# Performance work log

Measured on AMD Instinct MI355X. Metric: run time of the kernel, lower is better.

The kernel has to match this reference:

```python
import jax, jax.numpy as jnp
import numpy as np
from jax import lax

# SparseLSTM(input_size=1024, hidden_size=1024, blocks=4, density=0.5)
# input segments: width 512 at starts [0,170,341,512] (overlapping)
# output segments: contiguous quarters of 256
K = 4
IB = 512   # per-block input width
HB = 256   # per-block hidden width
STARTS = (0, 170, 341, 512)


def setup_inputs() -> dict:
    key = jax.random.key(0)
    ks = jax.random.split(key, 8)
    T, B, D = 512, 64, 1024
    std = 1.0 / np.sqrt(HB)
    return {
        "x":  jax.random.normal(ks[0], (T, B, D), jnp.float32),
        "h0": jax.random.normal(ks[1], (1, B, D), jnp.float32),
        "c0": jax.random.normal(ks[2], (1, B, D), jnp.float32),
        # stacked per-block LSTM params, PyTorch gate order (i, f, g, o)
        "W_ih": jax.random.uniform(ks[3], (K, 4 * HB, IB), jnp.float32, -std, std),
        "W_hh": jax.random.uniform(ks[4], (K, 4 * HB, HB), jnp.float32, -std, std),
        "b_ih": jax.random.uniform(ks[5], (K, 4 * HB), jnp.float32, -std, std),
        "b_hh": jax.random.uniform(ks[6], (K, 4 * HB), jnp.float32, -std, std),
    }


def _sparse_lstm(x, h0, c0, W_ih, W_hh, b_ih, b_hh):
    T, B, _ = x.shape
    # gather overlapping input slices -> [k, T, B, IB]
    xb = jnp.stack([lax.slice_in_dim(x, s, s + IB, axis=2) for s in STARTS])
    # contiguous hidden quarters -> [k, B, HB]
    hb = h0[0].reshape(B, K, HB).transpose(1, 0, 2)
    cb = c0[0].reshape(B, K, HB).transpose(1, 0, 2)
    # precompute input contributions to gates: [T, k, B, 4*HB]
    xg = jnp.einsum("ktbi,kgi->tkbg", xb, W_ih) + (b_ih + b_hh)[None, :, None, :]

    def step(carry, xg_t):
        h, c = carry  # each [k, B, HB]
        gates = xg_t + jnp.einsum("kbh,kgh->kbg", h, W_hh)
        i, f, g, o = jnp.split(gates, 4, axis=-1)
        c = jax.nn.sigmoid(f) * c + jax.nn.sigmoid(i) * jnp.tanh(g)
        h = jax.nn.sigmoid(o) * jnp.tanh(c)
        return (h, c), h

    (hT, cT), ys = lax.scan(step, (hb, cb), xg)  # ys: [T, k, B, HB]
    output = ys.transpose(0, 2, 1, 3).reshape(T, B, K * HB)
    new_h = hT.transpose(1, 0, 2).reshape(B, K * HB)[None]
    new_c = cT.transpose(1, 0, 2).reshape(B, K * HB)[None]
    return output, new_h, new_c


def reference(x, h0, c0, W_ih, W_hh, b_ih, b_hh):
    return _sparse_lstm(x, h0, c0, W_ih, W_hh, b_ih, b_hh)
```

## Files before the change

### kernel.cpp

```cpp
#include <hip/hip_runtime.h>

typedef _Float16 half8   __attribute__((ext_vector_type(8)));
typedef _Float16 half2_t __attribute__((ext_vector_type(2)));
typedef float    floatx4 __attribute__((ext_vector_type(4)));
typedef unsigned int uintx4 __attribute__((ext_vector_type(4)));
typedef unsigned int uint32;

__device__ __forceinline__ float sigm(float v) { return 1.0f / (1.0f + __expf(-v)); }
__device__ __forceinline__ float tanh_(float v) { float e = __expf(2.0f * v); return (e - 1.0f) / (e + 1.0f); }

__device__ __forceinline__ int dot4(uint32 a, uint32 b, int c) {
#if __has_builtin(__builtin_amdgcn_sdot4)
  return __builtin_amdgcn_sdot4((int)a, (int)b, c, false);
#else
  int r = c;
  r += (int)(char)(a)       * (int)(char)(b);
  r += (int)(char)(a >> 8)  * (int)(char)(b >> 8);
  r += (int)(char)(a >> 16) * (int)(char)(b >> 16);
  r += (int)(char)(a >> 24) * (int)(char)(b >> 24);
  return r;
#endif
}

__device__ __forceinline__ uint32 pack_rte(float a, float b) {
  half2_t h; h[0] = (_Float16)a; h[1] = (_Float16)b;
  return __builtin_bit_cast(uint32, h);
}

__global__ __launch_bounds__(256) void pack_wih(const float* __restrict__ wih, uint32* __restrict__ wihd) {
  int p = blockIdx.x * 256 + threadIdx.x;
  wihd[p] = pack_rte(wih[2 * p], wih[2 * p + 1]);
}

__global__ __launch_bounds__(256) void pack_whh8(const float* __restrict__ whh, uintx4* __restrict__ wq8) {
  int p = blockIdx.x * 256 + threadIdx.x;
  int row = p & 1023, qi = (p >> 10) & 3, qt = (p >> 12) & 3, kk = p >> 14;
  const float* src = whh + ((size_t)(kk * 1024 + row)) * 256 + qt * 64 + qi * 16;
  uint32 dw[4];
#pragma unroll
  for (int d = 0; d < 4; ++d) {
    uint32 v = 0;
#pragma unroll
    for (int e = 0; e < 4; ++e) {
      int q = (int)rintf(src[d * 4 + e] * 2032.0f);
      q = q > 127 ? 127 : (q < -127 ? -127 : q);
      v |= ((uint32)(q & 0xff)) << (8 * e);
    }
    dw[d] = v;
  }
  wq8[p] = (uintx4){dw[0], dw[1], dw[2], dw[3]};
}

__global__ __launch_bounds__(256) void pack_x_all(const float* __restrict__ x, uint32* __restrict__ xsd) {
  for (long p = (long)blockIdx.x * 256 + threadIdx.x; p < 33554432L; p += 2097152L) {
    int chunk = (int)(p >> 21);
    int r = (int)(p & 2097151);
    int k  = r >> 19;
    int R  = (r >> 8) & 2047;
    int pc = r & 255;
    int b = R >> 5, ct = R & 31;
    int t = chunk * 32 + ct;
    int sk = (k * 1024) / 6;
    const float* src = x + ((size_t)t * 64 + b) * 1024 + sk + pc * 2;
    xsd[p] = pack_rte(src[0], src[1]);
  }
}

__global__ __launch_bounds__(256) void gemm_all(const _Float16* __restrict__ xs,
                                                const _Float16* __restrict__ wih16,
                                                const float* __restrict__ bih,
                                                const float* __restrict__ bhh,
                                                _Float16* __restrict__ xg) {
  __shared__ _Float16 SL[18432];
  const int tid = threadIdx.x;
  const int bid = blockIdx.x;
  const int chunk = bid >> 9;
  const int b9 = bid & 511;
  const int nt = b9 & 7, mt = (b9 >> 3) & 15, kb = b9 >> 7;
  const int l = tid & 63;
  const int wid = tid >> 6;
  const int wm = wid >> 1, wn = wid & 1;
  const int lr = l & 15, lk = l >> 4;

  floatx4 acc[4][4] = {};
  const _Float16* xsk = xs + ((size_t)(chunk * 4 + kb) << 20);
  const _Float16* wk  = wih16 + ((size_t)kb << 19);

  for (int kt = 0; kt < 8; ++kt) {
    const int K0 = kt * 64;
    half8 av[4], bv[4];
#pragma unroll
    for (int q = 0; q < 4; ++q) {
      int s = q * 256 + tid;
      int row = s >> 3, c8 = s & 7;
      av[q] = *(const half8*)(xsk + (size_t)(mt * 128 + row) * 512 + K0 + c8 * 8);
      bv[q] = *(const half8*)(wk  + (size_t)(nt * 128 + row) * 512 + K0 + c8 * 8);
    }
#pragma unroll
    for (int q = 0; q < 4; ++q) {
      int s = q * 256 + tid;
      int row = s >> 3, c8 = s & 7;
      *(half8*)&SL[row * 72 + c8 * 8]        = av[q];
      *(half8*)&SL[9216 + row * 72 + c8 * 8] = bv[q];
    }
    __syncthreads();
#pragma unroll
    for (int ks = 0; ks < 2; ++ks) {
      half8 af[4], bf[4];
#pragma unroll
      for (int fm = 0; fm < 4; ++fm)
        af[fm] = *(const half8*)&SL[(wm * 64 + fm * 16 + lr) * 72 + (ks * 4 + lk) * 8];
#pragma unroll
      for (int fn = 0; fn < 4; ++fn)
        bf[fn] = *(const half8*)&SL[9216 + (wn * 64 + fn * 16 + lr) * 72 + (ks * 4 + lk) * 8];
#pragma unroll
      for (int fm = 0; fm < 4; ++fm)
#pragma unroll
        for (int fn = 0; fn < 4; ++fn)
          acc[fm][fn] = __builtin_amdgcn_mfma_f32_16x16x32_f16(af[fm], bf[fn], acc[fm][fn], 0, 0, 0);
    }
    __syncthreads();
  }
  float bias[4];
#pragma unroll
  for (int fn = 0; fn < 4; ++fn) {
    int g = nt * 128 + wn * 64 + fn * 16 + lr;
    bias[fn] = bih[kb * 1024 + g] + bhh[kb * 1024 + g];
  }
#pragma unroll
  for (int fm = 0; fm < 4; ++fm)
#pragma unroll
    for (int fn = 0; fn < 4; ++fn) {
      int colb = wn * 64 + fn * 16 + lr;
#pragma unroll
      for (int r = 0; r < 4; ++r) {
        int rowb = wm * 64 + fm * 16 + lk * 4 + r;
        SL[rowb * 128 + colb] = (_Float16)(acc[fm][fn][r] + bias[fn]);
      }
    }
  __syncthreads();
#pragma unroll
  for (int q = 0; q < 8; ++q) {
    int s = q * 256 + tid;
    int row = s >> 4, c16 = s & 15;
    int R = mt * 128 + row;
    size_t off = ((size_t)(kb * 64 + (R >> 5)) * 512 + chunk * 32 + (R & 31)) * 1024 + nt * 128 + c16 * 8;
    *(uintx4*)(xg + off) = *(const uintx4*)&SL[row * 128 + c16 * 8];
  }
}

__global__ __attribute__((amdgpu_flat_work_group_size(256, 256), amdgpu_waves_per_eu(1, 1)))
void lstm_all(const _Float16* __restrict__ xg,
              const uintx4* __restrict__ wq8,
              const float* __restrict__ h0,
              const float* __restrict__ c0,
              float* __restrict__ out) {
  extern __shared__ uint32 lds[];
  unsigned char* h8   = (unsigned char*)lds;
  _Float16*      hist = (_Float16*)(lds + 128);
  const _Float16* slab = (const _Float16*)(lds + 4224);
  const int j = threadIdx.x;
  const int k = blockIdx.x >> 6, b = blockIdx.x & 63;

  const uintx4* wb = wq8 + ((size_t)k << 14);
#define LW(g, i) uintx4 W##g##_##i = wb[((i) >> 2) * 4096 + ((i) & 3) * 1024 + (g) * 256 + j];
#define LWG(g) LW(g,0) LW(g,1) LW(g,2) LW(g,3) LW(g,4) LW(g,5) LW(g,6) LW(g,7) \
               LW(g,8) LW(g,9) LW(g,10) LW(g,11) LW(g,12) LW(g,13) LW(g,14) LW(g,15)
  LWG(0) LWG(1) LWG(2) LWG(3)
#undef LW
#undef LWG

  const int gi = b * 1024 + k * 256 + j;
  float cst = c0[gi];
  float hlast = h0[gi];
  {
    int q = (int)rintf(hlast * (127.0f / 8.0f));
    q = q > 127 ? 127 : (q < -127 ? -127 : q);
    h8[j] = (unsigned char)(q & 0xff);
  }

  const float DS1 = 0.0625f / 16129.0f;
  const float DS8 = 8.0f * DS1;

  const _Float16* xgp = xg + ((size_t)(k * 64 + b) << 19);

#define MACQ(W, H, d) { d = dot4(W[0], H[0], d); d = dot4(W[1], H[1], d); \
                        d = dot4(W[2], H[2], d); d = dot4(W[3], H[3], d); }
#define QSTEP(i) { uintx4 hq = hp[i]; \
    MACQ(W0_##i, hq, d0) MACQ(W1_##i, hq, d1) MACQ(W2_##i, hq, d2) MACQ(W3_##i, hq, d3) }

#pragma unroll 1
  for (int t = 0; t < 512; ++t) {
    if ((t & 31) == 0) {
      if (t) {
        int tb = t - 32;
#pragma unroll 1
        for (int q = 0; q < 32; ++q)
          out[((size_t)(tb + q) * 64 + b) * 1024 + k * 256 + j] = (float)hist[q * 256 + j];
      }
#pragma unroll
      for (int q = 0; q < 16; ++q)
        __builtin_amdgcn_global_load_lds(
            (const __attribute__((address_space(1))) void*)(xgp + (size_t)t * 1024 + q * 2048 + j * 8),
            (__attribute__((address_space(3))) void*)(lds + 4224 + q * 1024 + j * 4), 16, 0, 0);
      asm volatile("s_waitcnt vmcnt(0)" ::: "memory");
      __builtin_amdgcn_sched_barrier(0);
      __syncthreads();
    }

    const int cur = t & 1;
    const uintx4* hp = (const uintx4*)(h8 + cur * 256);
    int d0 = 0, d1 = 0, d2 = 0, d3 = 0;
    QSTEP(0)  QSTEP(1)  QSTEP(2)  QSTEP(3)  QSTEP(4)  QSTEP(5)  QSTEP(6)  QSTEP(7)
    QSTEP(8)  QSTEP(9)  QSTEP(10) QSTEP(11) QSTEP(12) QSTEP(13) QSTEP(14) QSTEP(15)

    const int ts = (t & 31) * 1024;
    float xi = (float)slab[ts + j];
    float xf = (float)slab[ts + 256 + j];
    float xgv = (float)slab[ts + 512 + j];
    float xo = (float)slab[ts + 768 + j];

    float dsc = (t == 0) ? DS8 : DS1;
    float iv = (float)d0 * dsc + xi;
    float fv = (float)d1 * dsc + xf;
    float gv = (float)d2 * dsc + xgv;
    float ov = (float)d3 * dsc + xo;
    float cn = sigm(fv) * cst + sigm(iv) * tanh_(gv);
    float hn = sigm(ov) * tanh_(cn);
    cst = cn; hlast = hn;
    hist[(t & 31) * 256 + j] = (_Float16)hn;
    {
      int q = (int)rintf(hn * 127.0f);
      h8[(cur ^ 1) * 256 + j] = (unsigned char)(q & 0xff);
    }
    __syncthreads();
  }
#undef MACQ
#undef QSTEP

#pragma unroll 1
  for (int q = 0; q < 32; ++q)
    out[((size_t)(480 + q) * 64 + b) * 1024 + k * 256 + j] = (float)hist[q * 256 + j];
  out[33554432 + gi] = hlast;
  out[33554432 + 65536 + gi] = cst;
}

extern "C" void kernel_launch(void* const* d_in, const int* in_sizes, int n_in,
                              void* d_out, int out_size, void* d_ws, size_t ws_size,
                              hipStream_t stream) {
  const float* x   = (const float*)d_in[0];
  const float* h0  = (const float*)d_in[1];
  const float* c0  = (const float*)d_in[2];
  const float* Wih = (const float*)d_in[3];
  const float* Whh = (const float*)d_in[4];
  const float* bih = (const float*)d_in[5];
  const float* bhh = (const float*)d_in[6];
  float* out = (float*)d_out;
  char* ws = (char*)d_ws;

  _Float16* xg16  = (_Float16*)ws;
  _Float16* xs    = (_Float16*)(ws + 268435456L);
  _Float16* wih16 = (_Float16*)(ws + 402653184L);
  uintx4*   wq8   = (uintx4*)(ws + 406847488L);

  hipFuncSetAttribute((const void*)lstm_all, hipFuncAttributeMaxDynamicSharedMemorySize, 82432);

  pack_wih<<<4096, 256, 0, stream>>>(Wih, (uint32*)wih16);
  pack_whh8<<<256, 256, 0, stream>>>(Whh, wq8);
  pack_x_all<<<8192, 256, 0, stream>>>(x, (uint32*)xs);
  gemm_all<<<8192, 256, 0, stream>>>(xs, wih16, bih, bhh, xg16);
  lstm_all<<<256, 256, 82432, stream>>>(xg16, wq8, h0, c0, out);
}
```

Measured before the change: 1.190 ms.

## Move recurrent weights partly to LDS and double-buffer small xg slabs

The recurrent kernel now keeps only one gate's int8 weights in registers, stages two gates plus part of the third in LDS (156 KB) and streams the rest of the third gate from global/L2 every step. The input-gate slab changes from a 32-step bulk load to a 4-step double-buffered prefetch, and hidden outputs are written straight to global memory each step instead of being batched through an LDS history buffer. The aim is to cut register pressure and the stalls from periodic bulk loads and flushes. In exchange, every step adds LDS and global weight reads on the serial critical path.

After: 1.953 ms. 1.64x slower.

```diff
diff --git a/kernel.cpp b/kernel.cpp
--- a/kernel.cpp
+++ b/kernel.cpp
@@ -149,7 +149,7 @@
   }
 }
 
-__global__ __attribute__((amdgpu_flat_work_group_size(256, 256), amdgpu_waves_per_eu(1, 1)))
+__global__ __launch_bounds__(256, 1)
 void lstm_all(const _Float16* __restrict__ xg,
               const uintx4* __restrict__ wq8,
               const float* __restrict__ h0,
@@ -157,68 +157,90 @@
               float* __restrict__ out) {
   extern __shared__ uint32 lds[];
   unsigned char* h8   = (unsigned char*)lds;
-  _Float16*      hist = (_Float16*)(lds + 128);
-  const _Float16* slab = (const _Float16*)(lds + 4224);
+  _Float16*      slab = (_Float16*)(lds + 128);
+  uintx4*        wl4  = (uintx4*)(lds + 4224);
   const int j = threadIdx.x;
   const int k = blockIdx.x >> 6, b = blockIdx.x & 63;
 
-  const uintx4* wb = wq8 + ((size_t)k << 14);
-#define LW(g, i) uintx4 W##g##_##i = wb[((i) >> 2) * 4096 + ((i) & 3) * 1024 + (g) * 256 + j];
-#define LWG(g) LW(g,0) LW(g,1) LW(g,2) LW(g,3) LW(g,4) LW(g,5) LW(g,6) LW(g,7) \
-               LW(g,8) LW(g,9) LW(g,10) LW(g,11) LW(g,12) LW(g,13) LW(g,14) LW(g,15)
-  LWG(0) LWG(1) LWG(2) LWG(3)
-#undef LW
-#undef LWG
+  const uintx4* wk = wq8 + ((size_t)k << 14);
+#define LR(i) uintx4 R##i = wk[((i) >> 2) * 4096 + ((i) & 3) * 1024 + j];
+  LR(0) LR(1) LR(2) LR(3) LR(4) LR(5) LR(6) LR(7)
+  LR(8) LR(9) LR(10) LR(11) LR(12) LR(13) LR(14) LR(15)
+#undef LR
+#pragma unroll
+  for (int g = 1; g <= 2; ++g)
+#pragma unroll
+    for (int i = 0; i < 16; ++i)
+      wl4[((g - 1) * 16 + i) * 256 + j] = wk[(i >> 2) * 4096 + (i & 3) * 1024 + g * 256 + j];
+  wl4[32 * 256 + j] = wk[768 + j];
+  wl4[33 * 256 + j] = wk[1024 + 768 + j];
+  const uintx4* w3 = wk + 768 + j;
 
   const int gi = b * 1024 + k * 256 + j;
   float cst = c0[gi];
-  float hlast = h0[gi];
+  float hn_prev = h0[gi];
   {
-    int q = (int)rintf(hlast * (127.0f / 8.0f));
+    int q = (int)rintf(hn_prev * (127.0f / 8.0f));
     q = q > 127 ? 127 : (q < -127 ? -127 : q);
     h8[j] = (unsigned char)(q & 0xff);
   }
 
+  const _Float16* xgp = xg + ((size_t)(k * 64 + b) << 19);
+#pragma unroll
+  for (int q = 0; q < 2; ++q) {
+    __builtin_amdgcn_global_load_lds(
+        (const __attribute__((address_space(1))) void*)(xgp + q * 2048 + j * 8),
+        (__attribute__((address_space(3))) void*)(lds + 128 + q * 1024 + j * 4), 16, 0, 0);
+    __builtin_amdgcn_global_load_lds(
+        (const __attribute__((address_space(1))) void*)(xgp + 4096 + q * 2048 + j * 8),
+        (__attribute__((address_space(3))) void*)(lds + 128 + 2048 + q * 1024 + j * 4), 16, 0, 0);
+  }
+  asm volatile("s_waitcnt vmcnt(0) lgkmcnt(0)" ::: "memory");
+  __builtin_amdgcn_sched_barrier(0);
+  __builtin_amdgcn_s_barrier();
+
   const float DS1 = 0.0625f / 16129.0f;
   const float DS8 = 8.0f * DS1;
 
-  const _Float16* xgp = xg + ((size_t)(k * 64 + b) << 19);
-
-#define MACQ(W, H, d) { d = dot4(W[0], H[0], d); d = dot4(W[1], H[1], d); \
-                        d = dot4(W[2], H[2], d); d = dot4(W[3], H[3], d); }
-#define QSTEP(i) { uintx4 hq = hp[i]; \
-    MACQ(W0_##i, hq, d0) MACQ(W1_##i, hq, d1) MACQ(W2_##i, hq, d2) MACQ(W3_##i, hq, d3) }
+#define MQ(W, H, d) { d = dot4(W[0], H[0], d); d = dot4(W[1], H[1], d); \
+                      d = dot4(W[2], H[2], d); d = dot4(W[3], H[3], d); }
+#define SI_L(i) { uintx4 hq = hp[i]; \
+    MQ(R##i, hq, d0) \
+    { uintx4 w = wl4[(i) * 256 + j];        MQ(w, hq, d1) } \
+    { uintx4 w = wl4[(16 + (i)) * 256 + j]; MQ(w, hq, d2) } \
+    { uintx4 w = wl4[(32 + (i)) * 256 + j]; MQ(w, hq, d3) } }
+#define SI_G(i) { uintx4 hq = hp[i]; \
+    MQ(R##i, hq, d0) \
+    { uintx4 w = wl4[(i) * 256 + j];        MQ(w, hq, d1) } \
+    { uintx4 w = wl4[(16 + (i)) * 256 + j]; MQ(w, hq, d2) } \
+    { uintx4 w = w3[((i) >> 2) * 4096 + ((i) & 3) * 1024]; MQ(w, hq, d3) } }
 
 #pragma unroll 1
   for (int t = 0; t < 512; ++t) {
-    if ((t & 31) == 0) {
-      if (t) {
-        int tb = t - 32;
-#pragma unroll 1
-        for (int q = 0; q < 32; ++q)
-          out[((size_t)(tb + q) * 64 + b) * 1024 + k * 256 + j] = (float)hist[q * 256 + j];
-      }
-#pragma unroll
-      for (int q = 0; q < 16; ++q)
-        __builtin_amdgcn_global_load_lds(
-            (const __attribute__((address_space(1))) void*)(xgp + (size_t)t * 1024 + q * 2048 + j * 8),
-            (__attribute__((address_space(3))) void*)(lds + 4224 + q * 1024 + j * 4), 16, 0, 0);
+    if ((t & 3) == 0 && t) {
       asm volatile("s_waitcnt vmcnt(0)" ::: "memory");
       __builtin_amdgcn_sched_barrier(0);
-      __syncthreads();
-    }
-
-    const int cur = t & 1;
-    const uintx4* hp = (const uintx4*)(h8 + cur * 256);
+      if (t + 4 < 512) {
+        const int nh = (((t >> 2) & 1) ^ 1);
+#pragma unroll
+        for (int q = 0; q < 2; ++q)
+          __builtin_amdgcn_global_load_lds(
+              (const __attribute__((address_space(1))) void*)(xgp + (size_t)(t + 4) * 1024 + q * 2048 + j * 8),
+              (__attribute__((address_space(3))) void*)(lds + 128 + nh * 2048 + q * 1024 + j * 4), 16, 0, 0);
+      }
+    }
+    const uintx4* hp = (const uintx4*)(h8 + (t & 1) * 256);
+    const _Float16* sl = slab + ((t >> 2) & 1) * 4096 + (t & 3) * 1024;
+
     int d0 = 0, d1 = 0, d2 = 0, d3 = 0;
-    QSTEP(0)  QSTEP(1)  QSTEP(2)  QSTEP(3)  QSTEP(4)  QSTEP(5)  QSTEP(6)  QSTEP(7)
-    QSTEP(8)  QSTEP(9)  QSTEP(10) QSTEP(11) QSTEP(12) QSTEP(13) QSTEP(14) QSTEP(15)
-
-    const int ts = (t & 31) * 1024;
-    float xi = (float)slab[ts + j];
-    float xf = (float)slab[ts + 256 + j];
-    float xgv = (float)slab[ts + 512 + j];
-    float xo = (float)slab[ts + 768 + j];
+    SI_L(0) SI_L(1)
+    SI_G(2) SI_G(3) SI_G(4) SI_G(5) SI_G(6) SI_G(7)
+    SI_G(8) SI_G(9) SI_G(10) SI_G(11) SI_G(12) SI_G(13) SI_G(14) SI_G(15)
+
+    float xi = (float)sl[j];
+    float xf = (float)sl[256 + j];
+    float xgv = (float)sl[512 + j];
+    float xo = (float)sl[768 + j];
 
     float dsc = (t == 0) ? DS8 : DS1;
     float iv = (float)d0 * dsc + xi;
@@ -227,21 +249,21 @@
     float ov = (float)d3 * dsc + xo;
     float cn = sigm(fv) * cst + sigm(iv) * tanh_(gv);
     float hn = sigm(ov) * tanh_(cn);
-    cst = cn; hlast = hn;
-    hist[(t & 31) * 256 + j] = (_Float16)hn;
+    cst = cn; hn_prev = hn;
+    out[((size_t)t * 64 + b) * 1024 + k * 256 + j] = hn;
     {
       int q = (int)rintf(hn * 127.0f);
-      h8[(cur ^ 1) * 256 + j] = (unsigned char)(q & 0xff);
-    }
-    __syncthreads();
-  }
-#undef MACQ
-#undef QSTEP
-
-#pragma unroll 1
-  for (int q = 0; q < 32; ++q)
-    out[((size_t)(480 + q) * 64 + b) * 1024 + k * 256 + j] = (float)hist[q * 256 + j];
-  out[33554432 + gi] = hlast;
+      h8[((t & 1) ^ 1) * 256 + j] = (unsigned char)(q & 0xff);
+    }
+    asm volatile("s_waitcnt lgkmcnt(0)" ::: "memory");
+    __builtin_amdgcn_sched_barrier(0);
+    __builtin_amdgcn_s_barrier();
+  }
+#undef MQ
+#undef SI_L
+#undef SI_G
+
+  out[33554432 + gi] = hn_prev;
   out[33554432 + 65536 + gi] = cst;
 }
 
@@ -263,11 +285,11 @@
   _Float16* wih16 = (_Float16*)(ws + 402653184L);
   uintx4*   wq8   = (uintx4*)(ws + 406847488L);
 
-  hipFuncSetAttribute((const void*)lstm_all, hipFuncAttributeMaxDynamicSharedMemorySize, 82432);
+  hipFuncSetAttribute((const void*)lstm_all, hipFuncAttributeMaxDynamicSharedMemorySize, 156160);
 
   pack_wih<<<4096, 256, 0, stream>>>(Wih, (uint32*)wih16);
   pack_whh8<<<256, 256, 0, stream>>>(Whh, wq8);
   pack_x_all<<<8192, 256, 0, stream>>>(x, (uint32*)xs);
   gemm_all<<<8192, 256, 0, stream>>>(xs, wih16, bih, bhh, xg16);
-  lstm_all<<<256, 256, 82432, stream>>>(xg16, wq8, h0, c0, out);
-}
+  lstm_all<<<256, 256, 156160, stream>>>(xg16, wq8, h0, c0, out);
+}
```

## Move half of recurrent weights to LDS and reload rest from global each step

Applied to the files above, without the earlier changes.

Instead of holding all 64 uintx4 int8 W_hh fragments per thread in registers, the forget and cell gate weights are staged once into LDS and the input and output gate weights are read from global memory (likely L1/L2 hits) on every timestep. The xg prefetch slab and output history are shrunk from 32-step to 8-step chunks, and the LDS allocation grows to hold the weight copy. This frees a large block of VGPRs, but it adds LDS and global load traffic inside the serial recurrence loop, so each step may get more latency-bound.

Result: slower. 1.287 ms (+8.1%).

```diff
diff --git a/kernel.cpp b/kernel.cpp
--- a/kernel.cpp
+++ b/kernel.cpp
@@ -149,7 +149,7 @@
   }
 }
 
-__global__ __attribute__((amdgpu_flat_work_group_size(256, 256), amdgpu_waves_per_eu(1, 1)))
+__global__ __launch_bounds__(256, 1)
 void lstm_all(const _Float16* __restrict__ xg,
               const uintx4* __restrict__ wq8,
               const float* __restrict__ h0,
@@ -157,24 +157,26 @@
               float* __restrict__ out) {
   extern __shared__ uint32 lds[];
   unsigned char* h8   = (unsigned char*)lds;
-  _Float16*      hist = (_Float16*)(lds + 128);
-  const _Float16* slab = (const _Float16*)(lds + 4224);
+  const _Float16* slab = (const _Float16*)(lds + 128);
+  _Float16*      hist = (_Float16*)(lds + 4224);
+  uintx4*        wl4  = (uintx4*)(lds + 5248);
   const int j = threadIdx.x;
   const int k = blockIdx.x >> 6, b = blockIdx.x & 63;
 
-  const uintx4* wb = wq8 + ((size_t)k << 14);
-#define LW(g, i) uintx4 W##g##_##i = wb[((i) >> 2) * 4096 + ((i) & 3) * 1024 + (g) * 256 + j];
-#define LWG(g) LW(g,0) LW(g,1) LW(g,2) LW(g,3) LW(g,4) LW(g,5) LW(g,6) LW(g,7) \
-               LW(g,8) LW(g,9) LW(g,10) LW(g,11) LW(g,12) LW(g,13) LW(g,14) LW(g,15)
-  LWG(0) LWG(1) LWG(2) LWG(3)
-#undef LW
-#undef LWG
+  const uintx4* wk = wq8 + ((size_t)k << 14);
+#pragma unroll
+  for (int i = 0; i < 16; ++i) {
+    wl4[i * 256 + j]        = wk[(i >> 2) * 4096 + (i & 3) * 1024 + 256 + j];
+    wl4[(16 + i) * 256 + j] = wk[(i >> 2) * 4096 + (i & 3) * 1024 + 512 + j];
+  }
+  const uintx4* w0s = wk + j;
+  const uintx4* w3s = wk + 768 + j;
 
   const int gi = b * 1024 + k * 256 + j;
   float cst = c0[gi];
-  float hlast = h0[gi];
+  float hn_prev = h0[gi];
   {
-    int q = (int)rintf(hlast * (127.0f / 8.0f));
+    int q = (int)rintf(hn_prev * (127.0f / 8.0f));
     q = q > 127 ? 127 : (q < -127 ? -127 : q);
     h8[j] = (unsigned char)(q & 0xff);
   }
@@ -184,37 +186,39 @@
 
   const _Float16* xgp = xg + ((size_t)(k * 64 + b) << 19);
 
-#define MACQ(W, H, d) { d = dot4(W[0], H[0], d); d = dot4(W[1], H[1], d); \
-                        d = dot4(W[2], H[2], d); d = dot4(W[3], H[3], d); }
-#define QSTEP(i) { uintx4 hq = hp[i]; \
-    MACQ(W0_##i, hq, d0) MACQ(W1_##i, hq, d1) MACQ(W2_##i, hq, d2) MACQ(W3_##i, hq, d3) }
+#define MQ(W, H, d) { d = dot4(W[0], H[0], d); d = dot4(W[1], H[1], d); \
+                      d = dot4(W[2], H[2], d); d = dot4(W[3], H[3], d); }
+#define STEPI(i) { uintx4 hq = hp[i]; \
+    { uintx4 w = w0s[((i) >> 2) * 4096 + ((i) & 3) * 1024]; MQ(w, hq, d0) } \
+    { uintx4 w = wl4[(i) * 256 + j];        MQ(w, hq, d1) } \
+    { uintx4 w = wl4[(16 + (i)) * 256 + j]; MQ(w, hq, d2) } \
+    { uintx4 w = w3s[((i) >> 2) * 4096 + ((i) & 3) * 1024]; MQ(w, hq, d3) } }
 
 #pragma unroll 1
   for (int t = 0; t < 512; ++t) {
-    if ((t & 31) == 0) {
+    if ((t & 7) == 0) {
       if (t) {
-        int tb = t - 32;
-#pragma unroll 1
-        for (int q = 0; q < 32; ++q)
+        int tb = t - 8;
+#pragma unroll
+        for (int q = 0; q < 8; ++q)
           out[((size_t)(tb + q) * 64 + b) * 1024 + k * 256 + j] = (float)hist[q * 256 + j];
       }
 #pragma unroll
-      for (int q = 0; q < 16; ++q)
+      for (int q = 0; q < 4; ++q)
         __builtin_amdgcn_global_load_lds(
             (const __attribute__((address_space(1))) void*)(xgp + (size_t)t * 1024 + q * 2048 + j * 8),
-            (__attribute__((address_space(3))) void*)(lds + 4224 + q * 1024 + j * 4), 16, 0, 0);
+            (__attribute__((address_space(3))) void*)(lds + 128 + q * 1024 + j * 4), 16, 0, 0);
       asm volatile("s_waitcnt vmcnt(0)" ::: "memory");
-      __builtin_amdgcn_sched_barrier(0);
       __syncthreads();
     }
 
     const int cur = t & 1;
     const uintx4* hp = (const uintx4*)(h8 + cur * 256);
     int d0 = 0, d1 = 0, d2 = 0, d3 = 0;
-    QSTEP(0)  QSTEP(1)  QSTEP(2)  QSTEP(3)  QSTEP(4)  QSTEP(5)  QSTEP(6)  QSTEP(7)
-    QSTEP(8)  QSTEP(9)  QSTEP(10) QSTEP(11) QSTEP(12) QSTEP(13) QSTEP(14) QSTEP(15)
-
-    const int ts = (t & 31) * 1024;
+    STEPI(0)  STEPI(1)  STEPI(2)  STEPI(3)  STEPI(4)  STEPI(5)  STEPI(6)  STEPI(7)
+    STEPI(8)  STEPI(9)  STEPI(10) STEPI(11) STEPI(12) STEPI(13) STEPI(14) STEPI(15)
+
+    const int ts = (t & 7) * 1024;
     float xi = (float)slab[ts + j];
     float xf = (float)slab[ts + 256 + j];
     float xgv = (float)slab[ts + 512 + j];
@@ -227,21 +231,21 @@
     float ov = (float)d3 * dsc + xo;
     float cn = sigm(fv) * cst + sigm(iv) * tanh_(gv);
     float hn = sigm(ov) * tanh_(cn);
-    cst = cn; hlast = hn;
-    hist[(t & 31) * 256 + j] = (_Float16)hn;
+    cst = cn; hn_prev = hn;
+    hist[(t & 7) * 256 + j] = (_Float16)hn;
     {
       int q = (int)rintf(hn * 127.0f);
       h8[(cur ^ 1) * 256 + j] = (unsigned char)(q & 0xff);
     }
     __syncthreads();
   }
-#undef MACQ
-#undef QSTEP
-
-#pragma unroll 1
-  for (int q = 0; q < 32; ++q)
-    out[((size_t)(480 + q) * 64 + b) * 1024 + k * 256 + j] = (float)hist[q * 256 + j];
-  out[33554432 + gi] = hlast;
+#undef MQ
+#undef STEPI
+
+#pragma unroll
+  for (int q = 0; q < 8; ++q)
+    out[((size_t)(504 + q) * 64 + b) * 1024 + k * 256 + j] = (float)hist[q * 256 + j];
+  out[33554432 + gi] = hn_prev;
   out[33554432 + 65536 + gi] = cst;
 }
 
@@ -263,11 +267,11 @@
   _Float16* wih16 = (_Float16*)(ws + 402653184L);
   uintx4*   wq8   = (uintx4*)(ws + 406847488L);
 
-  hipFuncSetAttribute((const void*)lstm_all, hipFuncAttributeMaxDynamicSharedMemorySize, 82432);
+  hipFuncSetAttribute((const void*)lstm_all, hipFuncAttributeMaxDynamicSharedMemorySize, 152064);
 
   pack_wih<<<4096, 256, 0, stream>>>(Wih, (uint32*)wih16);
   pack_whh8<<<256, 256, 0, stream>>>(Whh, wq8);
   pack_x_all<<<8192, 256, 0, stream>>>(x, (uint32*)xs);
   gemm_all<<<8192, 256, 0, stream>>>(xs, wih16, bih, bhh, xg16);
-  lstm_all<<<256, 256, 82432, stream>>>(xg16, wq8, h0, c0, out);
-}
+  lstm_all<<<256, 256, 152064, stream>>>(xg16, wq8, h0, c0, out);
+}
```
